# Performance work log

Hardware: AMD Instinct MI355X
Metric: run time of the kernel (lower is better)

Reference implementation:

```python
import jax, jax.numpy as jnp
import numpy as np

B, N, F, E, U, V = 64, 64, 512, 512, 1024, 32000  # batch, num_feature_vectors, feat_dim, embed_dim, units, vocab


def setup_inputs() -> dict:
    key = jax.random.key(0)
    ks = jax.random.split(key, 16)
    s = 0.05  # tf.random_normal_initializer default stddev
    return {
        "y": jax.random.randint(ks[0], (B, 1), 0, V),
        "features": jax.random.normal(ks[1], (B, N, F), jnp.float32),
        "state_output": jax.random.normal(ks[2], (B, U), jnp.float32),
        "h": jax.random.normal(ks[3], (B, U), jnp.float32),
        "c": jax.random.normal(ks[4], (B, U), jnp.float32),
        "Q": jax.random.normal(ks[5], (U, U), jnp.float32) * s,
        "K": jax.random.normal(ks[6], (U, N), jnp.float32) * s,
        "emb": jax.random.normal(ks[7], (V, E), jnp.float32) * 0.02,
        "W_x": jax.random.normal(ks[8], (F + E, 4 * U), jnp.float32) * 0.02,
        "W_h": jax.random.normal(ks[9], (U, 4 * U), jnp.float32) * 0.02,
        "b_lstm": jnp.zeros((4 * U,), jnp.float32),
        "W1": jax.random.normal(ks[10], (U, U), jnp.float32) * 0.02,
        "b1": jnp.zeros((U,), jnp.float32),
        "W2": jax.random.normal(ks[11], (U, V), jnp.float32) * 0.02,
        "b2": jnp.zeros((V,), jnp.float32),
    }


def reference(y, features, state_output, h, c, Q, K, emb, W_x, W_h, b_lstm, W1, b1, W2, b2):
    # DotProductAttention: per-example loop collapsed into one batched einsum.
    # w[b, n] = ((Q @ state^T)^T @ K)[b, n]  (same for every example i)
    w = (Q @ state_output.T).T @ K                      # [B, N]
    # loop body: aw[i] = w @ features[i]  -> stacked [B(i), B(b), F]
    aw = jnp.einsum('bn,inf->ibf', w, features)         # [B, B, F]
    aw = jax.nn.softmax(aw, axis=-1)                    # tf.nn.softmax default axis=-1
    context = jnp.sum(aw * features, axis=1)            # [B, F] (requires N == B)

    ye = emb[y[:, 0]]                                   # embedding + squeeze(axis=1): [B, E]
    x = jnp.concatenate([context, ye], axis=-1)         # [B, F+E]

    # Keras LSTMCell (gate order i, f, g, o)
    z = x @ W_x + h @ W_h + b_lstm                      # [B, 4U]
    zi, zf, zg, zo = jnp.split(z, 4, axis=-1)
    i_g = jax.nn.sigmoid(zi)
    f_g = jax.nn.sigmoid(zf)
    g_g = jnp.tanh(zg)
    o_g = jax.nn.sigmoid(zo)
    c_new = f_g * c + i_g * g_g
    h_new = o_g * jnp.tanh(c_new)

    logits = (h_new @ W1 + b1) @ W2 + b2                # fc1 (linear) -> fc2: [B, V]
    return logits, h_new, (h_new, c_new), aw
```

## Files before the change

### kernel.cpp

```cpp
#include <hip/hip_runtime.h>
#include <math.h>

#define WS_S    0
#define WS_W    65536
#define WS_CTX  69632
#define WS_YE   102400
#define WS_Z    135168
#define WS_T1   397312

#define OUT_LOGITS 0
#define OUT_H1     2048000
#define OUT_H2     2113536
#define OUT_C      2179072
#define OUT_AW     2244608

#define FMA4(ACC, A, W) { ACC.x += (A)*(W).x; ACC.y += (A)*(W).y; \
                          ACC.z += (A)*(W).z; ACC.w += (A)*(W).w; }

#define FMA_4ROW(WV) { \
    FMA4(acc[0], a0.x, WV) FMA4(acc[1], a0.y, WV) \
    FMA4(acc[2], a0.z, WV) FMA4(acc[3], a0.w, WV) }

__global__ __launch_bounds__(256) void k0_init(const int* __restrict__ y,
    const float* __restrict__ emb, const float* __restrict__ b_lstm,
    const float* __restrict__ b1, float* __restrict__ ws) {
  int idx = blockIdx.x * 256 + threadIdx.x;
  ws[WS_S + idx] = 0.f;
  ws[WS_T1 + idx] = b1[idx & 1023];
  *reinterpret_cast<float4*>(&ws[WS_Z + idx * 4]) =
      *reinterpret_cast<const float4*>(&b_lstm[(idx * 4) & 4095]);
  if (idx < 36864) ws[WS_W + idx] = 0.f;
  if (idx < 32768) {
    int b = idx >> 9, e = idx & 511;
    ws[WS_YE + idx] = emb[(size_t)y[b] * 512 + e];
  }
}

__global__ __launch_bounds__(256) void k1_sgemm(const float* __restrict__ so,
    const float* __restrict__ Q, float* __restrict__ ws) {
  __shared__ float Qt[64][65];
  __shared__ float SOt[64][68];
  int u0 = blockIdx.x * 64;
  int k0 = blockIdx.y * 64;
  int tid = threadIdx.x;
  for (int i = 0; i < 16; ++i) {
    int idx = tid + i * 256;
    int r = idx >> 6, k_l = idx & 63;
    Qt[k_l][r]  = Q[(u0 + r) * 1024 + k0 + k_l];
    SOt[k_l][r] = so[r * 1024 + k0 + k_l];
  }
  __syncthreads();
  int u = tid & 63, g = tid >> 6;
  float acc[16];
#pragma unroll
  for (int j = 0; j < 16; ++j) acc[j] = 0.f;
  for (int k_l = 0; k_l < 64; ++k_l) {
    float qv = Qt[k_l][u];
    const float4* sp = reinterpret_cast<const float4*>(&SOt[k_l][g * 16]);
    float4 s0 = sp[0], s1 = sp[1], s2 = sp[2], s3 = sp[3];
    acc[0]  += s0.x * qv; acc[1]  += s0.y * qv; acc[2]  += s0.z * qv; acc[3]  += s0.w * qv;
    acc[4]  += s1.x * qv; acc[5]  += s1.y * qv; acc[6]  += s1.z * qv; acc[7]  += s1.w * qv;
    acc[8]  += s2.x * qv; acc[9]  += s2.y * qv; acc[10] += s2.z * qv; acc[11] += s2.w * qv;
    acc[12] += s3.x * qv; acc[13] += s3.y * qv; acc[14] += s3.z * qv; acc[15] += s3.w * qv;
  }
  float* s_out = ws + WS_S;
#pragma unroll
  for (int j = 0; j < 16; ++j)
    atomicAdd(&s_out[(g * 16 + j) * 1024 + u0 + u], acc[j]);
}

__global__ __launch_bounds__(256) void k2_wgemm(const float* __restrict__ Katt,
    float* __restrict__ ws) {
  __shared__ float St[64][68];
  __shared__ float Kl[64][65];
  int k0 = blockIdx.x * 64;
  int tid = threadIdx.x;
  const float* s_in = ws + WS_S;
  for (int i = 0; i < 16; ++i) {
    int idx = tid + i * 256;
    int r = idx >> 6, q = idx & 63;
    St[q][r] = s_in[r * 1024 + k0 + q];
    Kl[r][q] = Katt[(k0 + r) * 64 + q];
  }
  __syncthreads();
  int n = tid & 63, g = tid >> 6;
  float acc[16];
#pragma unroll
  for (int j = 0; j < 16; ++j) acc[j] = 0.f;
  for (int k_l = 0; k_l < 64; ++k_l) {
    float kv = Kl[k_l][n];
    const float4* sp = reinterpret_cast<const float4*>(&St[k_l][g * 16]);
    float4 s0 = sp[0], s1 = sp[1], s2 = sp[2], s3 = sp[3];
    acc[0]  += s0.x * kv; acc[1]  += s0.y * kv; acc[2]  += s0.z * kv; acc[3]  += s0.w * kv;
    acc[4]  += s1.x * kv; acc[5]  += s1.y * kv; acc[6]  += s1.z * kv; acc[7]  += s1.w * kv;
    acc[8]  += s2.x * kv; acc[9]  += s2.y * kv; acc[10] += s2.z * kv; acc[11] += s2.w * kv;
    acc[12] += s3.x * kv; acc[13] += s3.y * kv; acc[14] += s3.z * kv; acc[15] += s3.w * kv;
  }
  float* w_out = ws + WS_W;
#pragma unroll
  for (int j = 0; j < 16; ++j)
    atomicAdd(&w_out[(g * 16 + j) * 64 + n], acc[j]);
}

__global__ __launch_bounds__(256) void k3_attn(const float* __restrict__ feat,
    float* __restrict__ ws, float* __restrict__ out) {
  __shared__ float wt[64][8];
  __shared__ float red[32];
  int i = blockIdx.x;
  int b0 = blockIdx.y * 8;
  int tid = threadIdx.x;
  int lane = tid & 63, wid = tid >> 6;
  const float* w_g = ws + WS_W;
  for (int t = tid; t < 512; t += 256) {
    int j = t >> 6, n = t & 63;
    wt[n][j] = w_g[(b0 + j) * 64 + n];
  }
  __syncthreads();
  const float* fi = feat + i * 32768;
  int f0 = tid * 2;
  float2 sc[8];
#pragma unroll
  for (int j = 0; j < 8; ++j) sc[j] = make_float2(0.f, 0.f);
  for (int n = 0; n < 64; n += 8) {
    float2 fv[8];
#pragma unroll
    for (int t = 0; t < 8; ++t)
      fv[t] = *reinterpret_cast<const float2*>(&fi[(n + t) * 512 + f0]);
#pragma unroll
    for (int t = 0; t < 8; ++t) {
      const float4* wp = reinterpret_cast<const float4*>(&wt[n + t][0]);
      float4 w0 = wp[0], w1 = wp[1];
      sc[0].x += w0.x * fv[t].x; sc[0].y += w0.x * fv[t].y;
      sc[1].x += w0.y * fv[t].x; sc[1].y += w0.y * fv[t].y;
      sc[2].x += w0.z * fv[t].x; sc[2].y += w0.z * fv[t].y;
      sc[3].x += w0.w * fv[t].x; sc[3].y += w0.w * fv[t].y;
      sc[4].x += w1.x * fv[t].x; sc[4].y += w1.x * fv[t].y;
      sc[5].x += w1.y * fv[t].x; sc[5].y += w1.y * fv[t].y;
      sc[6].x += w1.z * fv[t].x; sc[6].y += w1.z * fv[t].y;
      sc[7].x += w1.w * fv[t].x; sc[7].y += w1.w * fv[t].y;
    }
  }
  float m[8];
#pragma unroll
  for (int j = 0; j < 8; ++j) m[j] = fmaxf(sc[j].x, sc[j].y);
  for (int d = 1; d < 64; d <<= 1) {
#pragma unroll
    for (int j = 0; j < 8; ++j) m[j] = fmaxf(m[j], __shfl_xor(m[j], d));
  }
  if (lane == 0) {
#pragma unroll
    for (int j = 0; j < 8; ++j) red[wid * 8 + j] = m[j];
  }
  __syncthreads();
#pragma unroll
  for (int j = 0; j < 8; ++j)
    m[j] = fmaxf(fmaxf(red[j], red[8 + j]), fmaxf(red[16 + j], red[24 + j]));
  __syncthreads();
  float sm[8];
#pragma unroll
  for (int j = 0; j < 8; ++j) {
    sc[j].x = __expf(sc[j].x - m[j]);
    sc[j].y = __expf(sc[j].y - m[j]);
    sm[j] = sc[j].x + sc[j].y;
  }
  for (int d = 1; d < 64; d <<= 1) {
#pragma unroll
    for (int j = 0; j < 8; ++j) sm[j] += __shfl_xor(sm[j], d);
  }
  if (lane == 0) {
#pragma unroll
    for (int j = 0; j < 8; ++j) red[wid * 8 + j] = sm[j];
  }
  __syncthreads();
#pragma unroll
  for (int j = 0; j < 8; ++j)
    sm[j] = (red[j] + red[8 + j]) + (red[16 + j] + red[24 + j]);
  float2 ctx = make_float2(0.f, 0.f);
#pragma unroll
  for (int j = 0; j < 8; ++j) {
    float is = 1.f / sm[j];
    float ax = sc[j].x * is, ay = sc[j].y * is;
    *reinterpret_cast<float2*>(&out[OUT_AW + (i * 64 + b0 + j) * 512 + f0]) =
        make_float2(ax, ay);
    float2 fb = *reinterpret_cast<const float2*>(&fi[(b0 + j) * 512 + f0]);
    ctx.x += ax * fb.x;
    ctx.y += ay * fb.y;
  }
  float* ctxp = ws + WS_CTX + i * 512 + f0;
  atomicAdd(&ctxp[0], ctx.x);
  atomicAdd(&ctxp[1], ctx.y);
}

__global__ __launch_bounds__(256) void k5_zgemm(const float* __restrict__ h,
    const float* __restrict__ Wx, const float* __restrict__ Wh,
    float* __restrict__ ws) {
  __shared__ float At[128][68];
  int n0 = blockIdx.x * 64;
  int k0b = blockIdx.y * 256;
  int tid = threadIdx.x;
  int ng = tid & 15, g = tid >> 4;
  float4 acc[4];
#pragma unroll
  for (int j = 0; j < 4; ++j) acc[j] = make_float4(0.f, 0.f, 0.f, 0.f);
  for (int s = 0; s < 2; ++s) {
    int kc = k0b + s * 128;
    const float* src; int stride; int koff;
    if (kc < 512)       { src = ws + WS_CTX; stride = 512;  koff = kc; }
    else if (kc < 1024) { src = ws + WS_YE;  stride = 512;  koff = kc - 512; }
    else                { src = h;           stride = 1024; koff = kc - 1024; }
    if (s) __syncthreads();
    for (int it = 0; it < 32; ++it) {
      int idx = tid + it * 256;
      int k_l = idx & 127, b = idx >> 7;
      At[k_l][b] = src[b * stride + koff + k_l];
    }
    __syncthreads();
    const float* wp = ((kc < 1024) ? (Wx + (size_t)kc * 4096)
                                   : (Wh + (size_t)(kc - 1024) * 4096))
                      + n0 + ng * 4;
    float4 wv0[8], wv1[8];
#pragma unroll
    for (int t = 0; t < 8; ++t)
      wv0[t] = *reinterpret_cast<const float4*>(wp + (size_t)t * 4096);
    for (int kb = 0; kb < 128; kb += 16) {
#pragma unroll
      for (int t = 0; t < 8; ++t)
        wv1[t] = *reinterpret_cast<const float4*>(wp + (size_t)(kb + 8 + t) * 4096);
#pragma unroll
      for (int t = 0; t < 8; ++t) {
        float4 a0 = *reinterpret_cast<const float4*>(&At[kb + t][g * 4]);
        FMA_4ROW(wv0[t])
      }
      if (kb + 16 < 128) {
#pragma unroll
        for (int t = 0; t < 8; ++t)
          wv0[t] = *reinterpret_cast<const float4*>(wp + (size_t)(kb + 16 + t) * 4096);
      }
#pragma unroll
      for (int t = 0; t < 8; ++t) {
        float4 a0 = *reinterpret_cast<const float4*>(&At[kb + 8 + t][g * 4]);
        FMA_4ROW(wv1[t])
      }
    }
  }
  float* zp = ws + WS_Z + (size_t)(g * 4) * 4096 + n0 + ng * 4;
#pragma unroll
  for (int j = 0; j < 4; ++j) {
    atomicAdd(&zp[(size_t)j * 4096 + 0], acc[j].x);
    atomicAdd(&zp[(size_t)j * 4096 + 1], acc[j].y);
    atomicAdd(&zp[(size_t)j * 4096 + 2], acc[j].z);
    atomicAdd(&zp[(size_t)j * 4096 + 3], acc[j].w);
  }
}

__global__ __launch_bounds__(256) void k6_gates(const float* __restrict__ ws,
    const float* __restrict__ c, float* __restrict__ out) {
  int idx = blockIdx.x * 256 + threadIdx.x;
  int b = idx >> 10, u = idx & 1023;
  const float* z = ws + WS_Z;
  float zi = z[b * 4096 + u];
  float zf = z[b * 4096 + 1024 + u];
  float zg = z[b * 4096 + 2048 + u];
  float zo = z[b * 4096 + 3072 + u];
  float ig = 1.f / (1.f + __expf(-zi));
  float fg = 1.f / (1.f + __expf(-zf));
  float gg = tanhf(zg);
  float og = 1.f / (1.f + __expf(-zo));
  float cn = fg * c[idx] + ig * gg;
  float hn = og * tanhf(cn);
  out[OUT_H1 + idx] = hn;
  out[OUT_H2 + idx] = hn;
  out[OUT_C + idx] = cn;
}

__global__ __launch_bounds__(256) void k7_t1gemm(const float* __restrict__ out_r,
    const float* __restrict__ W1, float* __restrict__ ws) {
  __shared__ float At[64][68];
  int n0 = blockIdx.x * 64;
  int k0 = blockIdx.y * 64;
  int tid = threadIdx.x;
  const float* hn = out_r + OUT_H1;
  for (int it = 0; it < 16; ++it) {
    int idx = tid + it * 256;
    int k_l = idx & 63, b = idx >> 6;
    At[k_l][b] = hn[b * 1024 + k0 + k_l];
  }
  __syncthreads();
  int ng = tid & 15, g = tid >> 4;
  const float* wp = W1 + (size_t)k0 * 1024 + n0 + ng * 4;
  float4 acc[4];
#pragma unroll
  for (int j = 0; j < 4; ++j) acc[j] = make_float4(0.f, 0.f, 0.f, 0.f);
  for (int kb = 0; kb < 64; kb += 8) {
    float4 wv[8];
#pragma unroll
    for (int t = 0; t < 8; ++t)
      wv[t] = *reinterpret_cast<const float4*>(wp + (size_t)(kb + t) * 1024);
#pragma unroll
    for (int t = 0; t < 8; ++t) {
      float4 a0 = *reinterpret_cast<const float4*>(&At[kb + t][g * 4]);
      FMA4(acc[0], a0.x, wv[t]) FMA4(acc[1], a0.y, wv[t])
      FMA4(acc[2], a0.z, wv[t]) FMA4(acc[3], a0.w, wv[t])
    }
  }
  float* t1 = ws + WS_T1 + (size_t)(g * 4) * 1024 + n0 + ng * 4;
#pragma unroll
  for (int j = 0; j < 4; ++j) {
    atomicAdd(&t1[(size_t)j * 1024 + 0], acc[j].x);
    atomicAdd(&t1[(size_t)j * 1024 + 1], acc[j].y);
    atomicAdd(&t1[(size_t)j * 1024 + 2], acc[j].z);
    atomicAdd(&t1[(size_t)j * 1024 + 3], acc[j].w);
  }
}

__global__ __launch_bounds__(256) void k8_logits(const float* __restrict__ W2,
    const float* __restrict__ b2, const float* __restrict__ wsr,
    float* __restrict__ out) {
  __shared__ float At[128][68];
  int n0 = blockIdx.x * 64;
  int tid = threadIdx.x;
  int ng = tid & 15, g = tid >> 4;
  const float* t1 = wsr + WS_T1;
  float4 acc[4];
#pragma unroll
  for (int j = 0; j < 4; ++j) acc[j] = make_float4(0.f, 0.f, 0.f, 0.f);
  for (int kc = 0; kc < 1024; kc += 128) {
    if (kc) __syncthreads();
    for (int it = 0; it < 32; ++it) {
      int idx = tid + it * 256;
      int k_l = idx & 127, b = idx >> 7;
      At[k_l][b] = t1[b * 1024 + kc + k_l];
    }
    __syncthreads();
    const float* wp = W2 + (size_t)kc * 32000 + n0 + ng * 4;
    float4 wv0[8], wv1[8];
#pragma unroll
    for (int t = 0; t < 8; ++t)
      wv0[t] = *reinterpret_cast<const float4*>(wp + (size_t)t * 32000);
    for (int kb = 0; kb < 128; kb += 16) {
#pragma unroll
      for (int t = 0; t < 8; ++t)
        wv1[t] = *reinterpret_cast<const float4*>(wp + (size_t)(kb + 8 + t) * 32000);
#pragma unroll
      for (int t = 0; t < 8; ++t) {
        float4 a0 = *reinterpret_cast<const float4*>(&At[kb + t][g * 4]);
        FMA_4ROW(wv0[t])
      }
      if (kb + 16 < 128) {
#pragma unroll
        for (int t = 0; t < 8; ++t)
          wv0[t] = *reinterpret_cast<const float4*>(wp + (size_t)(kb + 16 + t) * 32000);
      }
#pragma unroll
      for (int t = 0; t < 8; ++t) {
        float4 a0 = *reinterpret_cast<const float4*>(&At[kb + 8 + t][g * 4]);
        FMA_4ROW(wv1[t])
      }
    }
  }
  float4 bias = *reinterpret_cast<const float4*>(b2 + n0 + ng * 4);
  float* op = out + OUT_LOGITS + (size_t)(g * 4) * 32000 + n0 + ng * 4;
#pragma unroll
  for (int j = 0; j < 4; ++j) {
    float4 v = acc[j];
    v.x += bias.x; v.y += bias.y; v.z += bias.z; v.w += bias.w;
    *reinterpret_cast<float4*>(&op[(size_t)j * 32000]) = v;
  }
}

extern "C" void kernel_launch(void* const* d_in, const int* in_sizes, int n_in,
                              void* d_out, int out_size, void* d_ws, size_t ws_size,
                              hipStream_t stream) {
  const int*   y    = (const int*)  d_in[0];
  const float* feat = (const float*)d_in[1];
  const float* so   = (const float*)d_in[2];
  const float* h    = (const float*)d_in[3];
  const float* c    = (const float*)d_in[4];
  const float* Q    = (const float*)d_in[5];
  const float* Katt = (const float*)d_in[6];
  const float* emb  = (const float*)d_in[7];
  const float* Wx   = (const float*)d_in[8];
  const float* Wh   = (const float*)d_in[9];
  const float* bl   = (const float*)d_in[10];
  const float* W1   = (const float*)d_in[11];
  const float* b1   = (const float*)d_in[12];
  const float* W2   = (const float*)d_in[13];
  const float* b2   = (const float*)d_in[14];
  float* ws  = (float*)d_ws;
  float* out = (float*)d_out;

  k0_init  <<<256, 256, 0, stream>>>(y, emb, bl, b1, ws);
  k1_sgemm <<<dim3(16, 16), 256, 0, stream>>>(so, Q, ws);
  k2_wgemm <<<16, 256, 0, stream>>>(Katt, ws);
  k3_attn  <<<dim3(64, 8), 256, 0, stream>>>(feat, ws, out);
  k5_zgemm <<<dim3(64, 8), 256, 0, stream>>>(h, Wx, Wh, ws);
  k6_gates <<<256, 256, 0, stream>>>(ws, c, out);
  k7_t1gemm<<<dim3(16, 16), 256, 0, stream>>>(out, W1, ws);
  k8_logits<<<500, 256, 0, stream>>>(W2, b2, ws, out);
}
```

Before: 438.3 us.

## Widen GEMM tiles to 16x4 per thread and split-K logits with atomics

```diff
diff --git a/kernel.cpp b/kernel.cpp
--- a/kernel.cpp
+++ b/kernel.cpp
@@ -17,9 +17,15 @@
 #define FMA4(ACC, A, W) { ACC.x += (A)*(W).x; ACC.y += (A)*(W).y; \
                           ACC.z += (A)*(W).z; ACC.w += (A)*(W).w; }
 
-#define FMA_4ROW(WV) { \
-    FMA4(acc[0], a0.x, WV) FMA4(acc[1], a0.y, WV) \
-    FMA4(acc[2], a0.z, WV) FMA4(acc[3], a0.w, WV) }
+#define FMA16(WV, A0, A1, A2, A3) { \
+    FMA4(acc[0],  A0.x, WV) FMA4(acc[1],  A0.y, WV) \
+    FMA4(acc[2],  A0.z, WV) FMA4(acc[3],  A0.w, WV) \
+    FMA4(acc[4],  A1.x, WV) FMA4(acc[5],  A1.y, WV) \
+    FMA4(acc[6],  A1.z, WV) FMA4(acc[7],  A1.w, WV) \
+    FMA4(acc[8],  A2.x, WV) FMA4(acc[9],  A2.y, WV) \
+    FMA4(acc[10], A2.z, WV) FMA4(acc[11], A2.w, WV) \
+    FMA4(acc[12], A3.x, WV) FMA4(acc[13], A3.y, WV) \
+    FMA4(acc[14], A3.z, WV) FMA4(acc[15], A3.w, WV) }
 
 __global__ __launch_bounds__(256) void k0_init(const int* __restrict__ y,
     const float* __restrict__ emb, const float* __restrict__ b_lstm,
@@ -36,6 +42,16 @@
   }
 }
 
+__global__ __launch_bounds__(256) void kb2_init(const float* __restrict__ b2,
+    float* __restrict__ out) {
+  int n = blockIdx.x * 256 + threadIdx.x;
+  int r0 = blockIdx.y * 16;
+  float v = b2[n];
+  float* p = out + OUT_LOGITS + (size_t)r0 * 32000 + n;
+#pragma unroll
+  for (int r = 0; r < 16; ++r) p[(size_t)r * 32000] = v;
+}
+
 __global__ __launch_bounds__(256) void k1_sgemm(const float* __restrict__ so,
     const float* __restrict__ Q, float* __restrict__ ws) {
   __shared__ float Qt[64][65];
@@ -195,57 +211,55 @@
     const float* __restrict__ Wx, const float* __restrict__ Wh,
     float* __restrict__ ws) {
   __shared__ float At[128][68];
-  int n0 = blockIdx.x * 64;
-  int k0b = blockIdx.y * 256;
-  int tid = threadIdx.x;
-  int ng = tid & 15, g = tid >> 4;
-  float4 acc[4];
-#pragma unroll
-  for (int j = 0; j < 4; ++j) acc[j] = make_float4(0.f, 0.f, 0.f, 0.f);
-  for (int s = 0; s < 2; ++s) {
-    int kc = k0b + s * 128;
-    const float* src; int stride; int koff;
-    if (kc < 512)       { src = ws + WS_CTX; stride = 512;  koff = kc; }
-    else if (kc < 1024) { src = ws + WS_YE;  stride = 512;  koff = kc - 512; }
-    else                { src = h;           stride = 1024; koff = kc - 1024; }
-    if (s) __syncthreads();
-    for (int it = 0; it < 32; ++it) {
-      int idx = tid + it * 256;
-      int k_l = idx & 127, b = idx >> 7;
-      At[k_l][b] = src[b * stride + koff + k_l];
-    }
-    __syncthreads();
-    const float* wp = ((kc < 1024) ? (Wx + (size_t)kc * 4096)
-                                   : (Wh + (size_t)(kc - 1024) * 4096))
-                      + n0 + ng * 4;
-    float4 wv0[8], wv1[8];
+  int n0 = blockIdx.x * 256;
+  int kc = blockIdx.y * 128;
+  int tid = threadIdx.x;
+  int lane = tid & 63, r0 = (tid >> 6) * 16;
+  const float* src; int stride; int koff;
+  if (kc < 512)       { src = ws + WS_CTX; stride = 512;  koff = kc; }
+  else if (kc < 1024) { src = ws + WS_YE;  stride = 512;  koff = kc - 512; }
+  else                { src = h;           stride = 1024; koff = kc - 1024; }
+  for (int it = 0; it < 32; ++it) {
+    int idx = tid + it * 256;
+    int k_l = idx & 127, b = idx >> 7;
+    At[k_l][b] = src[b * stride + koff + k_l];
+  }
+  __syncthreads();
+  const float* wp = ((kc < 1024) ? (Wx + (size_t)kc * 4096)
+                                 : (Wh + (size_t)(kc - 1024) * 4096))
+                    + n0 + lane * 4;
+  float4 acc[16];
+#pragma unroll
+  for (int j = 0; j < 16; ++j) acc[j] = make_float4(0.f, 0.f, 0.f, 0.f);
+  float4 wv0[8], wv1[8];
+#pragma unroll
+  for (int t = 0; t < 8; ++t)
+    wv0[t] = *reinterpret_cast<const float4*>(wp + (size_t)t * 4096);
+  for (int kb = 0; kb < 128; kb += 16) {
 #pragma unroll
     for (int t = 0; t < 8; ++t)
-      wv0[t] = *reinterpret_cast<const float4*>(wp + (size_t)t * 4096);
-    for (int kb = 0; kb < 128; kb += 16) {
+      wv1[t] = *reinterpret_cast<const float4*>(wp + (size_t)(kb + 8 + t) * 4096);
+#pragma unroll
+    for (int t = 0; t < 8; ++t) {
+      const float4* ap = reinterpret_cast<const float4*>(&At[kb + t][r0]);
+      float4 a0 = ap[0], a1 = ap[1], a2 = ap[2], a3 = ap[3];
+      FMA16(wv0[t], a0, a1, a2, a3)
+    }
+    if (kb + 16 < 128) {
 #pragma unroll
       for (int t = 0; t < 8; ++t)
-        wv1[t] = *reinterpret_cast<const float4*>(wp + (size_t)(kb + 8 + t) * 4096);
-#pragma unroll
-      for (int t = 0; t < 8; ++t) {
-        float4 a0 = *reinterpret_cast<const float4*>(&At[kb + t][g * 4]);
-        FMA_4ROW(wv0[t])
-      }
-      if (kb + 16 < 128) {
-#pragma unroll
-        for (int t = 0; t < 8; ++t)
-          wv0[t] = *reinterpret_cast<const float4*>(wp + (size_t)(kb + 16 + t) * 4096);
-      }
-#pragma unroll
-      for (int t = 0; t < 8; ++t) {
-        float4 a0 = *reinterpret_cast<const float4*>(&At[kb + 8 + t][g * 4]);
-        FMA_4ROW(wv1[t])
-      }
-    }
-  }
-  float* zp = ws + WS_Z + (size_t)(g * 4) * 4096 + n0 + ng * 4;
-#pragma unroll
-  for (int j = 0; j < 4; ++j) {
+        wv0[t] = *reinterpret_cast<const float4*>(wp + (size_t)(kb + 16 + t) * 4096);
+    }
+#pragma unroll
+    for (int t = 0; t < 8; ++t) {
+      const float4* ap = reinterpret_cast<const float4*>(&At[kb + 8 + t][r0]);
+      float4 a0 = ap[0], a1 = ap[1], a2 = ap[2], a3 = ap[3];
+      FMA16(wv1[t], a0, a1, a2, a3)
+    }
+  }
+  float* zp = ws + WS_Z + (size_t)r0 * 4096 + n0 + lane * 4;
+#pragma unroll
+  for (int j = 0; j < 16; ++j) {
     atomicAdd(&zp[(size_t)j * 4096 + 0], acc[j].x);
     atomicAdd(&zp[(size_t)j * 4096 + 1], acc[j].y);
     atomicAdd(&zp[(size_t)j * 4096 + 2], acc[j].z);
@@ -314,25 +328,26 @@
 }
 
 __global__ __launch_bounds__(256) void k8_logits(const float* __restrict__ W2,
-    const float* __restrict__ b2, const float* __restrict__ wsr,
-    float* __restrict__ out) {
+    const float* __restrict__ wsr, float* __restrict__ out) {
   __shared__ float At[128][68];
-  int n0 = blockIdx.x * 64;
-  int tid = threadIdx.x;
-  int ng = tid & 15, g = tid >> 4;
+  int n0 = blockIdx.x * 256;
+  int k0b = blockIdx.y * 256;
+  int tid = threadIdx.x;
+  int lane = tid & 63, r0 = (tid >> 6) * 16;
   const float* t1 = wsr + WS_T1;
-  float4 acc[4];
-#pragma unroll
-  for (int j = 0; j < 4; ++j) acc[j] = make_float4(0.f, 0.f, 0.f, 0.f);
-  for (int kc = 0; kc < 1024; kc += 128) {
-    if (kc) __syncthreads();
+  float4 acc[16];
+#pragma unroll
+  for (int j = 0; j < 16; ++j) acc[j] = make_float4(0.f, 0.f, 0.f, 0.f);
+  for (int s = 0; s < 2; ++s) {
+    int kc = k0b + s * 128;
+    if (s) __syncthreads();
     for (int it = 0; it < 32; ++it) {
       int idx = tid + it * 256;
       int k_l = idx & 127, b = idx >> 7;
       At[k_l][b] = t1[b * 1024 + kc + k_l];
     }
     __syncthreads();
-    const float* wp = W2 + (size_t)kc * 32000 + n0 + ng * 4;
+    const float* wp = W2 + (size_t)kc * 32000 + n0 + lane * 4;
     float4 wv0[8], wv1[8];
 #pragma unroll
     for (int t = 0; t < 8; ++t)
@@ -343,8 +358,9 @@
         wv1[t] = *reinterpret_cast<const float4*>(wp + (size_t)(kb + 8 + t) * 32000);
 #pragma unroll
       for (int t = 0; t < 8; ++t) {
-        float4 a0 = *reinterpret_cast<const float4*>(&At[kb + t][g * 4]);
-        FMA_4ROW(wv0[t])
+        const float4* ap = reinterpret_cast<const float4*>(&At[kb + t][r0]);
+        float4 a0 = ap[0], a1 = ap[1], a2 = ap[2], a3 = ap[3];
+        FMA16(wv0[t], a0, a1, a2, a3)
       }
       if (kb + 16 < 128) {
 #pragma unroll
@@ -353,18 +369,19 @@
       }
 #pragma unroll
       for (int t = 0; t < 8; ++t) {
-        float4 a0 = *reinterpret_cast<const float4*>(&At[kb + 8 + t][g * 4]);
-        FMA_4ROW(wv1[t])
+        const float4* ap = reinterpret_cast<const float4*>(&At[kb + 8 + t][r0]);
+        float4 a0 = ap[0], a1 = ap[1], a2 = ap[2], a3 = ap[3];
+        FMA16(wv1[t], a0, a1, a2, a3)
       }
     }
   }
-  float4 bias = *reinterpret_cast<const float4*>(b2 + n0 + ng * 4);
-  float* op = out + OUT_LOGITS + (size_t)(g * 4) * 32000 + n0 + ng * 4;
-#pragma unroll
-  for (int j = 0; j < 4; ++j) {
-    float4 v = acc[j];
-    v.x += bias.x; v.y += bias.y; v.z += bias.z; v.w += bias.w;
-    *reinterpret_cast<float4*>(&op[(size_t)j * 32000]) = v;
+  float* op = out + OUT_LOGITS + (size_t)r0 * 32000 + n0 + lane * 4;
+#pragma unroll
+  for (int j = 0; j < 16; ++j) {
+    atomicAdd(&op[(size_t)j * 32000 + 0], acc[j].x);
+    atomicAdd(&op[(size_t)j * 32000 + 1], acc[j].y);
+    atomicAdd(&op[(size_t)j * 32000 + 2], acc[j].z);
+    atomicAdd(&op[(size_t)j * 32000 + 3], acc[j].w);
   }
 }
 
@@ -390,11 +407,12 @@
   float* out = (float*)d_out;
 
   k0_init  <<<256, 256, 0, stream>>>(y, emb, bl, b1, ws);
+  kb2_init <<<dim3(125, 4), 256, 0, stream>>>(b2, out);
   k1_sgemm <<<dim3(16, 16), 256, 0, stream>>>(so, Q, ws);
   k2_wgemm <<<16, 256, 0, stream>>>(Katt, ws);
   k3_attn  <<<dim3(64, 8), 256, 0, stream>>>(feat, ws, out);
-  k5_zgemm <<<dim3(64, 8), 256, 0, stream>>>(h, Wx, Wh, ws);
+  k5_zgemm <<<dim3(16, 16), 256, 0, stream>>>(h, Wx, Wh, ws);
   k6_gates <<<256, 256, 0, stream>>>(ws, c, out);
   k7_t1gemm<<<dim3(16, 16), 256, 0, stream>>>(out, W1, ws);
-  k8_logits<<<500, 256, 0, stream>>>(W2, b2, ws, out);
-}
+  k8_logits<<<dim3(125, 4), 256, 0, stream>>>(W2, ws, out);
+}
```

Result: slower. 511.2 us (+16.6%).
